# Optimization experiments

Measured on AMD Instinct MI355X. Metric: run time of the kernel, lower is better.

## Reference

```python
import jax, jax.numpy as jnp
import numpy as np

LEAKY = 0.2     # PyG GATConv leaky_relu negative slope
BN_EPS = 1e-5

N, E, F_IN = 100000, 1600000, 7
ENC, HID, HEADS = 64, 32, 4
HC = HID * HEADS          # 128
DEC_IN, OUT = 64, 4
N_HIDDEN = 2              # nb_hidden_layers - 1


def gat_conv(z, src, dst, W, a_src, a_dst, b, concat):
    # PyG GATConv (shared lin for src/dst), dropout in eval mode = identity.
    n = z.shape[0]
    H, C = a_src.shape
    h = (z @ W).reshape(n, H, C)                      # [N,H,C]
    al_s = jnp.einsum('nhc,hc->nh', h, a_src)         # [N,H]
    al_d = jnp.einsum('nhc,hc->nh', h, a_dst)
    e = jax.nn.leaky_relu(al_s[src] + al_d[dst], LEAKY)   # [E,H]
    m = jax.ops.segment_max(e, dst, num_segments=n)       # scatter-softmax over in-edges
    ex = jnp.exp(e - m[dst])
    denom = jax.ops.segment_sum(ex, dst, num_segments=n)
    alpha = ex / (denom[dst] + 1e-16)                     # [E,H]
    out = jax.ops.segment_sum(h[src] * alpha[:, :, None], dst, num_segments=n)  # [N,H,C]
    out = out.reshape(n, H * C) if concat else out.mean(axis=1)
    return out + b


def batch_norm(z, gamma, beta):
    # track_running_stats=False -> always use batch statistics (biased var)
    mu = z.mean(axis=0)
    var = z.var(axis=0)
    return gamma * (z - mu) * jax.lax.rsqrt(var + BN_EPS) + beta


def setup_inputs() -> dict:
    key = jax.random.key(0)
    ks = jax.random.split(key, 20)
    g = lambda k, shape, fan: jax.random.normal(k, shape, jnp.float32) * (1.0 / np.sqrt(fan))
    inp = {
        'x': jax.random.normal(ks[0], (N, F_IN), jnp.float32),
        'edge_index': jax.random.randint(ks[1], (2, E), 0, N, jnp.int32),
        'enc_W': g(ks[2], (F_IN, ENC), F_IN),
        'enc_b': jnp.zeros((ENC,), jnp.float32),
        'in_W': g(ks[3], (ENC, HC), ENC),
        'in_att_src': g(ks[4], (HEADS, HID), HID),
        'in_att_dst': g(ks[5], (HEADS, HID), HID),
        'in_b': jnp.zeros((HC,), jnp.float32),
        'hid_W': g(ks[6], (N_HIDDEN, HC, HC), HC),
        'hid_att_src': g(ks[7], (N_HIDDEN, HEADS, HID), HID),
        'hid_att_dst': g(ks[8], (N_HIDDEN, HEADS, HID), HID),
        'hid_b': jnp.zeros((N_HIDDEN, HC), jnp.float32),
        'bn_gamma': jnp.ones((1 + N_HIDDEN, HC), jnp.float32),
        'bn_beta': jnp.zeros((1 + N_HIDDEN, HC), jnp.float32),
        'out_W': g(ks[9], (HC, DEC_IN), HC),           # out heads=1, concat=False
        'out_att_src': g(ks[10], (1, DEC_IN), DEC_IN),
        'out_att_dst': g(ks[11], (1, DEC_IN), DEC_IN),
        'out_b': jnp.zeros((DEC_IN,), jnp.float32),
        'dec_W': g(ks[12], (DEC_IN, OUT), DEC_IN),
        'dec_b': jnp.zeros((OUT,), jnp.float32),
    }
    return inp


def reference(x, edge_index, enc_W, enc_b, in_W, in_att_src, in_att_dst, in_b,
              hid_W, hid_att_src, hid_att_dst, hid_b, bn_gamma, bn_beta,
              out_W, out_att_src, out_att_dst, out_b, dec_W, dec_b):
    n = x.shape[0]
    loops = jnp.arange(n, dtype=edge_index.dtype)      # PyG GATConv add_self_loops=True
    src = jnp.concatenate([edge_index[0], loops])
    dst = jnp.concatenate([edge_index[1], loops])

    z = x @ enc_W + enc_b                              # encoder
    z = gat_conv(z, src, dst, in_W, in_att_src, in_att_dst, in_b, concat=True)
    z = jax.nn.relu(batch_norm(z, bn_gamma[0], bn_beta[0]))
    for i in range(N_HIDDEN):
        z = gat_conv(z, src, dst, hid_W[i], hid_att_src[i], hid_att_dst[i], hid_b[i], concat=True)
        z = jax.nn.relu(batch_norm(z, bn_gamma[i + 1], bn_beta[i + 1]))
    z = gat_conv(z, src, dst, out_W, out_att_src, out_att_dst, out_b, concat=False)
    z = z @ dec_W + dec_b                              # decoder
    return z
```

## Files before the change

kernel.cpp:

```cpp
#include <hip/hip_runtime.h>
#include <math.h>

#define LEAKY 0.2f
#define BN_EPS 1e-5f

typedef unsigned short u16;
typedef __bf16 bf16x8 __attribute__((ext_vector_type(8)));
typedef float f32x4 __attribute__((ext_vector_type(4)));
typedef u16 ushort8 __attribute__((ext_vector_type(8)));

__device__ __forceinline__ u16 f2bf(float x){
    unsigned u = __float_as_uint(x);
    u += 0x7FFFu + ((u >> 16) & 1u);
    return (u16)(u >> 16);
}
__device__ __forceinline__ float bf2f(u16 b){ return __uint_as_float(((unsigned)b) << 16); }


__global__ __launch_bounds__(256) void k_encoder(const float* __restrict__ x,
        const float* __restrict__ W, const float* __restrict__ b,
        float* __restrict__ z, int N){
    int gid = blockIdx.x*256 + threadIdx.x;
    int n = gid >> 6, j = gid & 63;
    if (n >= N) return;
    float acc = b[j];
    #pragma unroll
    for (int k=0;k<7;k++) acc += x[n*7+k]*W[k*64+j];
    z[(size_t)n*64+j] = acc;
}

template<int K, int MW, int MT>
__global__ __launch_bounds__(256) void k_pack_w(const float* __restrict__ W,
        u16* __restrict__ hi, u16* __restrict__ lo){
    int idx = blockIdx.x*256 + threadIdx.x;
    if (idx >= K*MW) return;
    int e = idx & 7, l16 = (idx >> 3) & 3, rest = idx >> 5;
    int n = rest % MW, t = rest / MW;
    int k = t*32 + l16*8 + e;
    float w = W[(size_t)k*MW + n];
    u16 hb = f2bf(w);
    size_t o = ((size_t)(t*MT + n)*4 + (size_t)l16)*8 + e;
    hi[o] = hb;
    lo[o] = f2bf(w - bf2f(hb));
}

template<int K, int MW, int MT, int H, int C>
__global__ __launch_bounds__(256) void k_pack_a(const float* __restrict__ W,
        const float* __restrict__ as, const float* __restrict__ ad,
        u16* __restrict__ hi, u16* __restrict__ lo){
    int idx = blockIdx.x*256 + threadIdx.x;
    if (idx >= K*16) return;
    int e = idx & 7, l16 = (idx >> 3) & 3, rest = idx >> 5;
    int j = rest % 16, t = rest / 16;
    int k = t*32 + l16*8 + e;
    float v = 0.f;
    if (j < 2*H){
        int hh = j >> 1;
        const float* a = (j & 1) ? ad : as;
        for (int c = 0; c < C; c++)
            v += W[(size_t)k*MW + hh*C + c] * a[hh*C + c];
    }
    u16 hb = f2bf(v);
    size_t o = ((size_t)(t*MT + MW + j)*4 + (size_t)l16)*8 + e;
    hi[o] = hb;
    lo[o] = f2bf(v - bf2f(hb));
}

__global__ void k_bn_coef(const float* __restrict__ cs, const float* __restrict__ cq,
        const float* __restrict__ g, const float* __restrict__ be,
        float* __restrict__ scale, float* __restrict__ shift, float invN){
    int j = threadIdx.x;
    float mu = cs[j]*invN;
    float var = cq[j]*invN - mu*mu;
    float s = g[j]*rsqrtf(var + BN_EPS);
    scale[j] = s; shift[j] = be[j] - mu*s;
}


template<int H>
__global__ __launch_bounds__(256) void k_mh1(const float* __restrict__ al,
        float* __restrict__ pm, int total){
    int t = threadIdx.x;
    float m = -1e30f;
    for (int i = blockIdx.x*256 + t; i < total; i += 64*256)
        m = fmaxf(m, al[i]);
    #pragma unroll
    for (int off = H; off < 64; off <<= 1)
        m = fmaxf(m, __shfl_xor(m, off, 64));
    __shared__ float ws[16];
    int lane = t & 63, wid = t >> 6;
    if (lane < H) ws[wid*H + lane] = m;
    __syncthreads();
    if (t < H){
        float mm = ws[t];
        #pragma unroll
        for (int w = 1; w < 4; w++) mm = fmaxf(mm, ws[w*H + t]);
        pm[blockIdx.x*H + t] = mm;
    }
}

template<int H>
__global__ void k_mh2(const float* __restrict__ pm, float* __restrict__ mh){
    int t = threadIdx.x;
    float m = -1e30f;
    #pragma unroll
    for (int k = 0; k < H; k++) m = fmaxf(m, pm[t + k*64]);
    #pragma unroll
    for (int off = H; off < 64; off <<= 1)
        m = fmaxf(m, __shfl_xor(m, off, 64));
    if (t < H) mh[t] = m;
}

template<int K, int MW, int RW, int CW, int WR, int WC, int H, bool BNIN>
__global__ __launch_bounds__(256) void k_gemm(const float* __restrict__ z,
        const u16* __restrict__ Whi, const u16* __restrict__ Wlo,
        const float* __restrict__ bnscale, const float* __restrict__ bnshift,
        u16* __restrict__ hout, float* __restrict__ al_s, float* __restrict__ al_d,
        int N)
{
    static_assert(RW*CW == 4 && RW*WR*16 == 64 && CW*WC*16 == MW, "tile config");
    constexpr int MT = MW + 16;
    constexpr int KS = K/32;
    constexpr int KG = K/8;
    __shared__ __align__(16) u16 Ahi[64*K];
    __shared__ __align__(16) u16 Alo[64*K];
    const int brow = blockIdx.x*64;
    const int tid = threadIdx.x;

    for (int u = tid; u < 64*KG; u += 256){
        int row = u / KG, kg = u % KG;
        int gr = brow + row;
        float v[8];
        if (gr < N){
            const float4* p = (const float4*)(z + (size_t)gr*K + kg*8);
            float4 a = p[0], bq = p[1];
            v[0]=a.x; v[1]=a.y; v[2]=a.z; v[3]=a.w;
            v[4]=bq.x; v[5]=bq.y; v[6]=bq.z; v[7]=bq.w;
            if (BNIN){
                const float4* sc = (const float4*)(bnscale + kg*8);
                const float4* sh = (const float4*)(bnshift + kg*8);
                float4 s0=sc[0], s1=sc[1], t0=sh[0], t1=sh[1];
                v[0]=fmaxf(fmaf(v[0],s0.x,t0.x),0.f);
                v[1]=fmaxf(fmaf(v[1],s0.y,t0.y),0.f);
                v[2]=fmaxf(fmaf(v[2],s0.z,t0.z),0.f);
                v[3]=fmaxf(fmaf(v[3],s0.w,t0.w),0.f);
                v[4]=fmaxf(fmaf(v[4],s1.x,t1.x),0.f);
                v[5]=fmaxf(fmaf(v[5],s1.y,t1.y),0.f);
                v[6]=fmaxf(fmaf(v[6],s1.z,t1.z),0.f);
                v[7]=fmaxf(fmaf(v[7],s1.w,t1.w),0.f);
            }
        } else {
            #pragma unroll
            for (int e=0;e<8;e++) v[e]=0.f;
        }
        ushort8 h8, l8;
        #pragma unroll
        for (int e=0;e<8;e++){
            u16 hb = f2bf(v[e]);
            h8[e] = hb;
            l8[e] = f2bf(v[e] - bf2f(hb));
        }
        int rb = row >> 4, t = kg >> 2, lg = kg & 3;
        int gidx = (rb*KS + t)*64 + (row & 15) + 16*lg;
        gidx ^= (gidx >> 4) & 7;
        *(ushort8*)&Ahi[gidx*8] = h8;
        *(ushort8*)&Alo[gidx*8] = l8;
    }
    __syncthreads();

    const int wave = tid >> 6, lane = tid & 63;
    const int wrow = wave / CW, wcol = wave % CW;
    const int l15 = lane & 15, l16 = lane >> 4;

    f32x4 acc[WR][WC];
    f32x4 acc_e[WR];
    #pragma unroll
    for (int r=0;r<WR;r++){
        acc_e[r] = (f32x4){0.f,0.f,0.f,0.f};
        #pragma unroll
        for (int c=0;c<WC;c++) acc[r][c] = (f32x4){0.f,0.f,0.f,0.f};
    }

    #pragma unroll
    for (int t = 0; t < KS; ++t){
        bf16x8 ah[WR], al[WR];
        #pragma unroll
        for (int r=0;r<WR;r++){
            int rb = wrow*WR + r;
            int goff = (rb*KS + t)*64 + lane;
            goff ^= (goff >> 4) & 7;
            ah[r] = *(const bf16x8*)&Ahi[goff*8];
            al[r] = *(const bf16x8*)&Alo[goff*8];
        }
        bf16x8 bh[WC], bl[WC];
        #pragma unroll
        for (int c=0;c<WC;c++){
            int n = (wcol*WC + c)*16 + l15;
            size_t off = ((size_t)(t*MT + n)*4 + (size_t)l16)*8;
            bh[c] = *(const bf16x8*)&Whi[off];
            bl[c] = *(const bf16x8*)&Wlo[off];
        }
        #pragma unroll
        for (int r=0;r<WR;r++)
            #pragma unroll
            for (int c=0;c<WC;c++){
                acc[r][c] = __builtin_amdgcn_mfma_f32_16x16x32_bf16(al[r], bh[c], acc[r][c], 0,0,0);
                acc[r][c] = __builtin_amdgcn_mfma_f32_16x16x32_bf16(ah[r], bl[c], acc[r][c], 0,0,0);
                acc[r][c] = __builtin_amdgcn_mfma_f32_16x16x32_bf16(ah[r], bh[c], acc[r][c], 0,0,0);
            }
        if (wcol == 0){
            size_t offE = ((size_t)(t*MT + MW + l15)*4 + (size_t)l16)*8;
            bf16x8 bhe = *(const bf16x8*)&Whi[offE];
            bf16x8 ble = *(const bf16x8*)&Wlo[offE];
            #pragma unroll
            for (int r=0;r<WR;r++){
                acc_e[r] = __builtin_amdgcn_mfma_f32_16x16x32_bf16(al[r], bhe, acc_e[r], 0,0,0);
                acc_e[r] = __builtin_amdgcn_mfma_f32_16x16x32_bf16(ah[r], ble, acc_e[r], 0,0,0);
                acc_e[r] = __builtin_amdgcn_mfma_f32_16x16x32_bf16(ah[r], bhe, acc_e[r], 0,0,0);
            }
        }
    }

    if (wcol == 0 && l15 < 2*H){
        int j = l15;
        #pragma unroll
        for (int r=0;r<WR;r++)
            #pragma unroll
            for (int q=0;q<4;q++){
                int rowg = brow + (wrow*WR + r)*16 + l16*4 + q;
                if (rowg < N){
                    float v = acc_e[r][q];
                    if (H==4){
                        if (j & 1) al_d[(size_t)rowg*4 + (j>>1)] = v;
                        else       al_s[(size_t)rowg*4 + (j>>1)] = v;
                    } else {
                        if (j & 1) al_d[rowg] = v;
                        else       al_s[rowg] = v;
                    }
                }
            }
    }

    #pragma unroll
    for (int r=0;r<WR;r++)
        #pragma unroll
        for (int c=0;c<WC;c++){
            int colg = (wcol*WC + c)*16 + l15;
            #pragma unroll
            for (int q=0;q<4;q++){
                int rowg = brow + (wrow*WR + r)*16 + l16*4 + q;
                if (rowg < N) hout[(size_t)rowg*MW + colg] = f2bf(acc[r][c][q]);
            }
        }
}


__global__ __launch_bounds__(256) void k_deg(const int* __restrict__ ei, int E,
        int* __restrict__ deg){
    int e = blockIdx.x*256 + threadIdx.x;
    if (e < E) atomicAdd(deg + ei[E+e], 1);
}

__device__ __forceinline__ int wave_scan(int v, int lane){
    #pragma unroll
    for (int off=1; off<64; off<<=1){
        int t = __shfl_up(v, off, 64);
        if (lane >= off) v += t;
    }
    return v;
}

__global__ __launch_bounds__(1024) void k_scan1(const int* __restrict__ deg,
        int* __restrict__ excl, int* __restrict__ bsum, int N){
    __shared__ int ws[16];
    int i = blockIdx.x*1024 + threadIdx.x;
    int lane = threadIdx.x & 63, wid = threadIdx.x >> 6;
    int v = (i < N) ? deg[i] : 0;
    int inc = wave_scan(v, lane);
    if (lane == 63) ws[wid] = inc;
    __syncthreads();
    if (wid == 0){
        int wv = (lane < 16) ? ws[lane] : 0;
        int winc = wave_scan(wv, lane);
        if (lane < 16) ws[lane] = winc - wv;
    }
    __syncthreads();
    int off = ws[wid];
    if (i < N) excl[i] = off + inc - v;
    if (threadIdx.x == 1023) bsum[blockIdx.x] = off + inc;
}

__global__ void k_scan2(int* __restrict__ bsum, int nb){
    if (threadIdx.x == 0 && blockIdx.x == 0){
        int c = 0;
        for (int i = 0; i < nb; i++){ int t = bsum[i]; bsum[i] = c; c += t; }
    }
}

__global__ __launch_bounds__(256) void k_scan3(const int* __restrict__ excl,
        const int* __restrict__ bsum, int* __restrict__ rowptr,
        int* __restrict__ cursor, int N, int E){
    int i = blockIdx.x*256 + threadIdx.x;
    if (i < N){
        int r = excl[i] + bsum[i >> 10];
        rowptr[i] = r; cursor[i] = r;
    } else if (i == N){
        rowptr[N] = E;
    }
}

__global__ __launch_bounds__(256) void k_bucket(const int* __restrict__ ei, int E,
        int* __restrict__ cursor, int* __restrict__ csr){
    int e = blockIdx.x*256 + threadIdx.x;
    if (e >= E) return;
    int pos = atomicAdd(cursor + ei[E+e], 1);
    csr[pos] = ei[e];
}


template<int H, int C, bool STATS, bool DECODE>
__global__ __launch_bounds__(256) void k_gat_agg(
        const int* __restrict__ rowptr, const int* __restrict__ csr_src,
        const float* __restrict__ al_s, const float* __restrict__ al_d,
        const float* __restrict__ mh,
        const u16* __restrict__ hfeat, const float* __restrict__ b,
        float* __restrict__ z, float* __restrict__ cs, float* __restrict__ cq,
        const float* __restrict__ decW, const float* __restrict__ decb,
        float* __restrict__ out, int N, int totWaves)
{
    constexpr int M = H*C;
    constexpr int GS = M/8;
    constexpr int EPS = 64/GS;
    const int lane = threadIdx.x & 63;
    const int q = lane % GS;
    const int g = lane / GS;
    const int col0 = q*8;
    const int hd = col0 / C;
    const int gw = blockIdx.x*4 + (threadIdx.x >> 6);

    const float mhf = mh[hd];
    float bj[8];
    #pragma unroll
    for (int j=0;j<8;j++) bj[j] = b[col0+j];

    float w[8][4];
    if (DECODE){
        #pragma unroll
        for (int j=0;j<8;j++)
            #pragma unroll
            for (int o=0;o<4;o++) w[j][o] = decW[(col0+j)*4 + o];
    }
    float ls[8], lq[8];
    if (STATS){
        #pragma unroll
        for (int j=0;j<8;j++){ ls[j]=0.f; lq[j]=0.f; }
    }

    for (int dst = gw; dst < N; dst += totWaves){
        int p0 = rowptr[dst], p1 = rowptr[dst+1];
        float ald = al_d[(size_t)dst*H + hd];
        float v0 = al_s[(size_t)dst*H + hd] + ald;
        v0 = v0 > 0.f ? v0 : LEAKY*v0;
        float tt = mhf + ald;
        float mb = tt > 0.f ? tt : LEAKY*tt;
        mb = fminf(mb, v0 + 40.f);

        float ex0 = __expf(v0 - mb) * (1.0f/EPS);
        float s = ex0;
        float acc[8];
        ushort8 hd8 = *(const ushort8*)(hfeat + (size_t)dst*M + col0);
        #pragma unroll
        for (int j=0;j<8;j++) acc[j] = bf2f(hd8[j]) * ex0;

        auto LD = [&](int base, ushort8& hv, float& vs){
            int idx = base + g;
            int src = dst;
            if (idx < p1) src = csr_src[idx];
            float t = al_s[(size_t)src*H + hd];
            vs = (idx < p1) ? t : -1e30f;
            hv = *(const ushort8*)(hfeat + (size_t)src*M + col0);
        };
        auto PR = [&](const ushort8& hv, float vs){
            float vv = vs + ald;
            vv = vv > 0.f ? vv : LEAKY*vv;
            float ex = __expf(vv - mb);
            s += ex;
            #pragma unroll
            for (int j=0;j<8;j++) acc[j] = fmaf(bf2f(hv[j]), ex, acc[j]);
        };

        ushort8 hvA, hvB; float vsA=0.f, vsB=0.f;
        int p = p0;
        LD(p, hvA, vsA);
        while (p < p1){
            LD(p+EPS, hvB, vsB);
            PR(hvA, vsA);
            p += EPS;
            if (p >= p1) break;
            LD(p+EPS, hvA, vsA);
            PR(hvB, vsB);
            p += EPS;
        }

        #pragma unroll
        for (int off = GS; off < 64; off <<= 1){
            s += __shfl_xor(s, off, 64);
            #pragma unroll
            for (int j=0;j<8;j++) acc[j] += __shfl_xor(acc[j], off, 64);
        }
        float inv = 1.f/s;
        float o8[8];
        #pragma unroll
        for (int j=0;j<8;j++) o8[j] = acc[j]*inv + bj[j];

        if (STATS){
            #pragma unroll
            for (int j=0;j<8;j++){ ls[j] += o8[j]; lq[j] += o8[j]*o8[j]; }
        }
        if (!DECODE){
            if (lane < GS){
                f32x4 w0v = {o8[0],o8[1],o8[2],o8[3]};
                f32x4 w1v = {o8[4],o8[5],o8[6],o8[7]};
                __builtin_nontemporal_store(w0v, (f32x4*)(z + (size_t)dst*M + col0));
                __builtin_nontemporal_store(w1v, (f32x4*)(z + (size_t)dst*M + col0 + 4));
            }
        } else {
            float p4[4] = {0.f,0.f,0.f,0.f};
            #pragma unroll
            for (int j=0;j<8;j++)
                #pragma unroll
                for (int o=0;o<4;o++) p4[o] = fmaf(o8[j], w[j][o], p4[o]);
            #pragma unroll
            for (int off=1; off<GS; off<<=1){
                #pragma unroll
                for (int o=0;o<4;o++) p4[o] += __shfl_xor(p4[o], off, 64);
            }
            if (lane == 0){
                f32x4 o = {p4[0]+decb[0], p4[1]+decb[1], p4[2]+decb[2], p4[3]+decb[3]};
                __builtin_nontemporal_store(o, (f32x4*)(out + (size_t)dst*4));
            }
        }
    }

    if (STATS){
        __shared__ float sls[128], slq[128];
        if (threadIdx.x < 128){ sls[threadIdx.x]=0.f; slq[threadIdx.x]=0.f; }
        __syncthreads();
        if (lane < GS){
            #pragma unroll
            for (int j=0;j<8;j++){
                atomicAdd(&sls[col0+j], ls[j]);
                atomicAdd(&slq[col0+j], lq[j]);
            }
        }
        __syncthreads();
        if (threadIdx.x < 128){
            atomicAdd(cs + threadIdx.x, sls[threadIdx.x]);
            atomicAdd(cq + threadIdx.x, slq[threadIdx.x]);
        }
    }
}

extern "C" void kernel_launch(void* const* d_in, const int* in_sizes, int n_in,
                              void* d_out, int out_size, void* d_ws, size_t ws_size,
                              hipStream_t stream){
    const float* x      = (const float*)d_in[0];
    const int*   ei     = (const int*)  d_in[1];
    const float* enc_W  = (const float*)d_in[2];
    const float* enc_b  = (const float*)d_in[3];
    const float* in_W   = (const float*)d_in[4];
    const float* in_as  = (const float*)d_in[5];
    const float* in_ad  = (const float*)d_in[6];
    const float* in_b   = (const float*)d_in[7];
    const float* hid_W  = (const float*)d_in[8];
    const float* hid_as = (const float*)d_in[9];
    const float* hid_ad = (const float*)d_in[10];
    const float* hid_b  = (const float*)d_in[11];
    const float* bn_g   = (const float*)d_in[12];
    const float* bn_b   = (const float*)d_in[13];
    const float* out_W  = (const float*)d_in[14];
    const float* out_as = (const float*)d_in[15];
    const float* out_ad = (const float*)d_in[16];
    const float* out_b  = (const float*)d_in[17];
    const float* dec_W  = (const float*)d_in[18];
    const float* dec_b  = (const float*)d_in[19];

    const int N = in_sizes[0] / 7;
    const int E = in_sizes[1] / 2;
    const int NB = (N + 1023) / 1024;
    const int NT = (N + 63) / 64;
    const int AGG_BLOCKS = 2048, TOT_WAVES = AGG_BLOCKS*4;

    float*    bufZ   = (float*)d_ws;
    float*    al_s   = bufZ + (size_t)N*128;
    float*    al_d   = al_s + (size_t)N*4;
    float*    cs     = al_d + (size_t)N*4;
    float*    cq     = cs + 128;
    float*    mh     = cq + 128;
    float*    pm     = mh + 8;
    float*    scale  = pm + 256;
    float*    shift  = scale + 128;
    int*      deg    = (int*)(shift + 128);
    int*      excl   = deg + N;
    int*      rowptr = excl + N;
    int*      cursor = rowptr + (N+1);
    int*      bsum   = cursor + N;
    int*      csr    = bsum + NB;
    u16*      hb     = (u16*)(((uintptr_t)(csr + E) + 15) & ~(uintptr_t)15);
    u16*      wk     = hb + (size_t)N*128;
    u16* wk_in_hi  = wk;                     u16* wk_in_lo  = wk_in_hi  + 64*144;
    u16* wk_h0_hi  = wk_in_lo  + 64*144;     u16* wk_h0_lo  = wk_h0_hi  + 128*144;
    u16* wk_h1_hi  = wk_h0_lo  + 128*144;    u16* wk_h1_lo  = wk_h1_hi  + 128*144;
    u16* wk_out_hi = wk_h1_lo  + 128*144;    u16* wk_out_lo = wk_out_hi + 128*80;

    k_pack_w<64,128,144><<<(64*128+255)/256, 256, 0, stream>>>(in_W, wk_in_hi, wk_in_lo);
    k_pack_a<64,128,144,4,32><<<(64*16+255)/256, 256, 0, stream>>>(in_W, in_as, in_ad, wk_in_hi, wk_in_lo);
    k_pack_w<128,128,144><<<(128*128+255)/256, 256, 0, stream>>>(hid_W, wk_h0_hi, wk_h0_lo);
    k_pack_a<128,128,144,4,32><<<(128*16+255)/256, 256, 0, stream>>>(hid_W, hid_as, hid_ad, wk_h0_hi, wk_h0_lo);
    k_pack_w<128,128,144><<<(128*128+255)/256, 256, 0, stream>>>(hid_W + 128*128, wk_h1_hi, wk_h1_lo);
    k_pack_a<128,128,144,4,32><<<(128*16+255)/256, 256, 0, stream>>>(hid_W + 128*128, hid_as + 128, hid_ad + 128, wk_h1_hi, wk_h1_lo);
    k_pack_w<128,64,80><<<(128*64+255)/256, 256, 0, stream>>>(out_W, wk_out_hi, wk_out_lo);
    k_pack_a<128,64,80,1,64><<<(128*16+255)/256, 256, 0, stream>>>(out_W, out_as, out_ad, wk_out_hi, wk_out_lo);

    hipMemsetAsync(deg, 0, (size_t)N*sizeof(int), stream);
    k_deg   <<<(E+255)/256, 256, 0, stream>>>(ei, E, deg);
    k_scan1 <<<NB, 1024, 0, stream>>>(deg, excl, bsum, N);
    k_scan2 <<<1, 64, 0, stream>>>(bsum, NB);
    k_scan3 <<<(N+1+255)/256, 256, 0, stream>>>(excl, bsum, rowptr, cursor, N, E);
    k_bucket<<<(E+255)/256, 256, 0, stream>>>(ei, E, cursor, csr);

    k_encoder<<<(N*64+255)/256, 256, 0, stream>>>(x, enc_W, enc_b, bufZ, N);

    const float invN = 1.f/(float)N;

    hipMemsetAsync(cs, 0, 256*sizeof(float), stream);
    k_gemm<64,128,2,2,2,4,4,false><<<NT, 256, 0, stream>>>(bufZ, wk_in_hi, wk_in_lo,
            nullptr, nullptr, hb, al_s, al_d, N);
    k_mh1<4><<<64, 256, 0, stream>>>(al_s, pm, N*4);
    k_mh2<4><<<1, 64, 0, stream>>>(pm, mh);
    k_gat_agg<4,32,true,false><<<AGG_BLOCKS, 256, 0, stream>>>(rowptr, csr, al_s, al_d, mh,
            hb, in_b, bufZ, cs, cq, nullptr, nullptr, nullptr, N, TOT_WAVES);
    k_bn_coef<<<1, 128, 0, stream>>>(cs, cq, bn_g, bn_b, scale, shift, invN);

    for (int i = 0; i < 2; i++){
        const u16* whi = i ? wk_h1_hi : wk_h0_hi;
        const u16* wlo = i ? wk_h1_lo : wk_h0_lo;
        hipMemsetAsync(cs, 0, 256*sizeof(float), stream);
        k_gemm<128,128,2,2,2,4,4,true><<<NT, 256, 0, stream>>>(bufZ, whi, wlo,
                scale, shift, hb, al_s, al_d, N);
        k_mh1<4><<<64, 256, 0, stream>>>(al_s, pm, N*4);
        k_mh2<4><<<1, 64, 0, stream>>>(pm, mh);
        k_gat_agg<4,32,true,false><<<AGG_BLOCKS, 256, 0, stream>>>(rowptr, csr, al_s, al_d, mh,
                hb, hid_b + (size_t)i*128, bufZ, cs, cq, nullptr, nullptr, nullptr, N, TOT_WAVES);
        k_bn_coef<<<1, 128, 0, stream>>>(cs, cq, bn_g + (i+1)*128, bn_b + (i+1)*128, scale, shift, invN);
    }

    k_gemm<128,64,4,1,1,4,1,true><<<NT, 256, 0, stream>>>(bufZ, wk_out_hi, wk_out_lo,
            scale, shift, hb, al_s, al_d, N);
    k_mh1<1><<<64, 256, 0, stream>>>(al_s, pm, N);
    k_mh2<1><<<1, 64, 0, stream>>>(pm, mh);
    k_gat_agg<1,64,false,true><<<AGG_BLOCKS, 256, 0, stream>>>(rowptr, csr, al_s, al_d, mh,
            hb, out_b, nullptr, nullptr, nullptr, dec_W, dec_b, (float*)d_out, N, TOT_WAVES);
}
```

Baseline: 944.6 us.

## Fuse encoder into first GEMM and compute per-block alpha max in GEMM

The encoder linear layer is now computed inside the first GEMM's A-tile load from x and shared-memory encoder weights, so the 64-wide intermediate no longer goes through global memory. Each GEMM block also reduces the source-attention logits to a per-block maximum using an order-preserving integer atomicMax in shared memory. This replaces the two-kernel global max pass with a single small reduction kernel over NT*H partials. The cost is extra work and a barrier inside the GEMM, plus a larger pm buffer.

New measurement: 928.3 us. About the same (-1.7%).

```diff
diff --git a/kernel.cpp b/kernel.cpp
--- a/kernel.cpp
+++ b/kernel.cpp
@@ -16,17 +16,13 @@
 }
 __device__ __forceinline__ float bf2f(u16 b){ return __uint_as_float(((unsigned)b) << 16); }
 
-
-__global__ __launch_bounds__(256) void k_encoder(const float* __restrict__ x,
-        const float* __restrict__ W, const float* __restrict__ b,
-        float* __restrict__ z, int N){
-    int gid = blockIdx.x*256 + threadIdx.x;
-    int n = gid >> 6, j = gid & 63;
-    if (n >= N) return;
-    float acc = b[j];
-    #pragma unroll
-    for (int k=0;k<7;k++) acc += x[n*7+k]*W[k*64+j];
-    z[(size_t)n*64+j] = acc;
+__device__ __forceinline__ unsigned enc_ord(float x){
+    unsigned u = __float_as_uint(x);
+    return (u & 0x80000000u) ? ~u : (u | 0x80000000u);
+}
+__device__ __forceinline__ float dec_ord(unsigned u){
+    unsigned b = (u & 0x80000000u) ? (u ^ 0x80000000u) : ~u;
+    return __uint_as_float(b);
 }
 
 template<int K, int MW, int MT>
@@ -76,14 +72,11 @@
     scale[j] = s; shift[j] = be[j] - mu*s;
 }
 
-
 template<int H>
-__global__ __launch_bounds__(256) void k_mh1(const float* __restrict__ al,
-        float* __restrict__ pm, int total){
+__global__ void k_mh2b(const float* __restrict__ pm, float* __restrict__ mh, int total){
     int t = threadIdx.x;
     float m = -1e30f;
-    for (int i = blockIdx.x*256 + t; i < total; i += 64*256)
-        m = fmaxf(m, al[i]);
+    for (int i = t; i < total; i += 256) m = fmaxf(m, pm[i]);
     #pragma unroll
     for (int off = H; off < 64; off <<= 1)
         m = fmaxf(m, __shfl_xor(m, off, 64));
@@ -95,28 +88,18 @@
         float mm = ws[t];
         #pragma unroll
         for (int w = 1; w < 4; w++) mm = fmaxf(mm, ws[w*H + t]);
-        pm[blockIdx.x*H + t] = mm;
-    }
-}
-
-template<int H>
-__global__ void k_mh2(const float* __restrict__ pm, float* __restrict__ mh){
-    int t = threadIdx.x;
-    float m = -1e30f;
-    #pragma unroll
-    for (int k = 0; k < H; k++) m = fmaxf(m, pm[t + k*64]);
-    #pragma unroll
-    for (int off = H; off < 64; off <<= 1)
-        m = fmaxf(m, __shfl_xor(m, off, 64));
-    if (t < H) mh[t] = m;
-}
-
-template<int K, int MW, int RW, int CW, int WR, int WC, int H, bool BNIN>
+        mh[t] = mm;
+    }
+}
+
+template<int K, int MW, int RW, int CW, int WR, int WC, int H, bool BNIN, bool ENC>
 __global__ __launch_bounds__(256) void k_gemm(const float* __restrict__ z,
         const u16* __restrict__ Whi, const u16* __restrict__ Wlo,
         const float* __restrict__ bnscale, const float* __restrict__ bnshift,
+        const float* __restrict__ x, const float* __restrict__ encW,
+        const float* __restrict__ encb,
         u16* __restrict__ hout, float* __restrict__ al_s, float* __restrict__ al_d,
-        int N)
+        float* __restrict__ pm, int N)
 {
     static_assert(RW*CW == 4 && RW*WR*16 == 64 && CW*WC*16 == MW, "tile config");
     constexpr int MT = MW + 16;
@@ -124,30 +107,53 @@
     constexpr int KG = K/8;
     __shared__ __align__(16) u16 Ahi[64*K];
     __shared__ __align__(16) u16 Alo[64*K];
+    __shared__ unsigned smax[H];
+    __shared__ float sEnc[ENC ? 7*64 + 64 : 1];
     const int brow = blockIdx.x*64;
     const int tid = threadIdx.x;
+
+    if (ENC){
+        for (int i = tid; i < 7*64; i += 256) sEnc[i] = encW[i];
+        if (tid < 64) sEnc[7*64 + tid] = encb[tid];
+        __syncthreads();
+    }
+    if (tid < H) smax[tid] = 0;
 
     for (int u = tid; u < 64*KG; u += 256){
         int row = u / KG, kg = u % KG;
         int gr = brow + row;
         float v[8];
         if (gr < N){
-            const float4* p = (const float4*)(z + (size_t)gr*K + kg*8);
-            float4 a = p[0], bq = p[1];
-            v[0]=a.x; v[1]=a.y; v[2]=a.z; v[3]=a.w;
-            v[4]=bq.x; v[5]=bq.y; v[6]=bq.z; v[7]=bq.w;
-            if (BNIN){
-                const float4* sc = (const float4*)(bnscale + kg*8);
-                const float4* sh = (const float4*)(bnshift + kg*8);
-                float4 s0=sc[0], s1=sc[1], t0=sh[0], t1=sh[1];
-                v[0]=fmaxf(fmaf(v[0],s0.x,t0.x),0.f);
-                v[1]=fmaxf(fmaf(v[1],s0.y,t0.y),0.f);
-                v[2]=fmaxf(fmaf(v[2],s0.z,t0.z),0.f);
-                v[3]=fmaxf(fmaf(v[3],s0.w,t0.w),0.f);
-                v[4]=fmaxf(fmaf(v[4],s1.x,t1.x),0.f);
-                v[5]=fmaxf(fmaf(v[5],s1.y,t1.y),0.f);
-                v[6]=fmaxf(fmaf(v[6],s1.z,t1.z),0.f);
-                v[7]=fmaxf(fmaf(v[7],s1.w,t1.w),0.f);
+            if (ENC){
+                float xr[7];
+                #pragma unroll
+                for (int k=0;k<7;k++) xr[k] = x[(size_t)gr*7 + k];
+                #pragma unroll
+                for (int e=0;e<8;e++){
+                    int j = kg*8 + e;
+                    float a = sEnc[7*64 + j];
+                    #pragma unroll
+                    for (int k=0;k<7;k++) a = fmaf(xr[k], sEnc[k*64 + j], a);
+                    v[e] = a;
+                }
+            } else {
+                const float4* p = (const float4*)(z + (size_t)gr*K + kg*8);
+                float4 a = p[0], bq = p[1];
+                v[0]=a.x; v[1]=a.y; v[2]=a.z; v[3]=a.w;
+                v[4]=bq.x; v[5]=bq.y; v[6]=bq.z; v[7]=bq.w;
+                if (BNIN){
+                    const float4* sc = (const float4*)(bnscale + kg*8);
+                    const float4* sh = (const float4*)(bnshift + kg*8);
+                    float4 s0=sc[0], s1=sc[1], t0=sh[0], t1=sh[1];
+                    v[0]=fmaxf(fmaf(v[0],s0.x,t0.x),0.f);
+                    v[1]=fmaxf(fmaf(v[1],s0.y,t0.y),0.f);
+                    v[2]=fmaxf(fmaf(v[2],s0.z,t0.z),0.f);
+                    v[3]=fmaxf(fmaf(v[3],s0.w,t0.w),0.f);
+                    v[4]=fmaxf(fmaf(v[4],s1.x,t1.x),0.f);
+                    v[5]=fmaxf(fmaf(v[5],s1.y,t1.y),0.f);
+                    v[6]=fmaxf(fmaf(v[6],s1.z,t1.z),0.f);
+                    v[7]=fmaxf(fmaf(v[7],s1.w,t1.w),0.f);
+                }
             }
         } else {
             #pragma unroll
@@ -223,6 +229,7 @@
 
     if (wcol == 0 && l15 < 2*H){
         int j = l15;
+        float wm = -1e30f;
         #pragma unroll
         for (int r=0;r<WR;r++)
             #pragma unroll
@@ -238,7 +245,13 @@
                         else       al_s[rowg] = v;
                     }
                 }
-            }
+                if (!(j & 1)) wm = fmaxf(wm, acc_e[r][q]);
+            }
+        if (!(j & 1)){
+            wm = fmaxf(wm, __shfl_xor(wm, 16, 64));
+            wm = fmaxf(wm, __shfl_xor(wm, 32, 64));
+            if (l16 == 0) atomicMax(&smax[j>>1], enc_ord(wm));
+        }
     }
 
     #pragma unroll
@@ -252,6 +265,9 @@
                 if (rowg < N) hout[(size_t)rowg*MW + colg] = f2bf(acc[r][c][q]);
             }
         }
+
+    __syncthreads();
+    if (tid < H) pm[(size_t)blockIdx.x*H + tid] = dec_ord(smax[tid]);
 }
 
 
@@ -498,7 +514,7 @@
     float*    cq     = cs + 128;
     float*    mh     = cq + 128;
     float*    pm     = mh + 8;
-    float*    scale  = pm + 256;
+    float*    scale  = pm + 8192;
     float*    shift  = scale + 128;
     int*      deg    = (int*)(shift + 128);
     int*      excl   = deg + N;
@@ -529,15 +545,12 @@
     k_scan3 <<<(N+1+255)/256, 256, 0, stream>>>(excl, bsum, rowptr, cursor, N, E);
     k_bucket<<<(E+255)/256, 256, 0, stream>>>(ei, E, cursor, csr);
 
-    k_encoder<<<(N*64+255)/256, 256, 0, stream>>>(x, enc_W, enc_b, bufZ, N);
-
     const float invN = 1.f/(float)N;
 
     hipMemsetAsync(cs, 0, 256*sizeof(float), stream);
-    k_gemm<64,128,2,2,2,4,4,false><<<NT, 256, 0, stream>>>(bufZ, wk_in_hi, wk_in_lo,
-            nullptr, nullptr, hb, al_s, al_d, N);
-    k_mh1<4><<<64, 256, 0, stream>>>(al_s, pm, N*4);
-    k_mh2<4><<<1, 64, 0, stream>>>(pm, mh);
+    k_gemm<64,128,2,2,2,4,4,false,true><<<NT, 256, 0, stream>>>(bufZ, wk_in_hi, wk_in_lo,
+            nullptr, nullptr, x, enc_W, enc_b, hb, al_s, al_d, pm, N);
+    k_mh2b<4><<<1, 256, 0, stream>>>(pm, mh, NT*4);
     k_gat_agg<4,32,true,false><<<AGG_BLOCKS, 256, 0, stream>>>(rowptr, csr, al_s, al_d, mh,
             hb, in_b, bufZ, cs, cq, nullptr, nullptr, nullptr, N, TOT_WAVES);
     k_bn_coef<<<1, 128, 0, stream>>>(cs, cq, bn_g, bn_b, scale, shift, invN);
@@ -546,19 +559,17 @@
         const u16* whi = i ? wk_h1_hi : wk_h0_hi;
         const u16* wlo = i ? wk_h1_lo : wk_h0_lo;
         hipMemsetAsync(cs, 0, 256*sizeof(float), stream);
-        k_gemm<128,128,2,2,2,4,4,true><<<NT, 256, 0, stream>>>(bufZ, whi, wlo,
-                scale, shift, hb, al_s, al_d, N);
-        k_mh1<4><<<64, 256, 0, stream>>>(al_s, pm, N*4);
-        k_mh2<4><<<1, 64, 0, stream>>>(pm, mh);
+        k_gemm<128,128,2,2,2,4,4,true,false><<<NT, 256, 0, stream>>>(bufZ, whi, wlo,
+                scale, shift, nullptr, nullptr, nullptr, hb, al_s, al_d, pm, N);
+        k_mh2b<4><<<1, 256, 0, stream>>>(pm, mh, NT*4);
         k_gat_agg<4,32,true,false><<<AGG_BLOCKS, 256, 0, stream>>>(rowptr, csr, al_s, al_d, mh,
                 hb, hid_b + (size_t)i*128, bufZ, cs, cq, nullptr, nullptr, nullptr, N, TOT_WAVES);
         k_bn_coef<<<1, 128, 0, stream>>>(cs, cq, bn_g + (i+1)*128, bn_b + (i+1)*128, scale, shift, invN);
     }
 
-    k_gemm<128,64,4,1,1,4,1,true><<<NT, 256, 0, stream>>>(bufZ, wk_out_hi, wk_out_lo,
-            scale, shift, hb, al_s, al_d, N);
-    k_mh1<1><<<64, 256, 0, stream>>>(al_s, pm, N);
-    k_mh2<1><<<1, 64, 0, stream>>>(pm, mh);
+    k_gemm<128,64,4,1,1,4,1,true,false><<<NT, 256, 0, stream>>>(bufZ, wk_out_hi, wk_out_lo,
+            scale, shift, nullptr, nullptr, nullptr, hb, al_s, al_d, pm, N);
+    k_mh2b<1><<<1, 256, 0, stream>>>(pm, mh, NT);
     k_gat_agg<1,64,false,true><<<AGG_BLOCKS, 256, 0, stream>>>(rowptr, csr, al_s, al_d, mh,
             hb, out_b, nullptr, nullptr, nullptr, dec_W, dec_b, (float*)d_out, N, TOT_WAVES);
 }
```
